# Kernel optimization log

Measured on AMD Instinct MI355X. Metric: run time of the kernel, lower is better.

## Reference

```python
import jax, jax.numpy as jnp
import numpy as np
import math

B, QL, HID = 4, 4, 4096          # batch, speculative q_len, hidden_size
NH, NKV, HD = 32, 8, 128         # attention heads, kv heads, head_dim
GROUPS = NH // NKV               # GQA repeat factor = 4
PRIOR = 4096                     # cached (prior) KV length
THETA = 1.0e6                    # Mixtral rope_theta


def setup_inputs() -> dict:
    key = jax.random.key(0)
    ks = jax.random.split(key, 7)
    hidden_states = jax.random.normal(ks[0], (B, QL, HID), jnp.float32)
    past_k = jax.random.normal(ks[1], (B, NKV, PRIOR, HD), jnp.float32)
    past_v = jax.random.normal(ks[2], (B, NKV, PRIOR, HD), jnp.float32)
    wq = jax.random.normal(ks[3], (HID, NH * HD), jnp.float32) * 0.02
    wk = jax.random.normal(ks[4], (HID, NKV * HD), jnp.float32) * 0.02
    wv = jax.random.normal(ks[5], (HID, NKV * HD), jnp.float32) * 0.02
    wo = jax.random.normal(ks[6], (NH * HD, HID), jnp.float32) * 0.02
    # prior mask: all cached positions visible
    attention_mask = jnp.ones((B, 1, QL, PRIOR), dtype=bool)
    # active mask: causal over the speculative window
    active_mask = jnp.broadcast_to(jnp.tril(jnp.ones((QL, QL), dtype=bool)), (B, 1, QL, QL))
    position_ids = jnp.broadcast_to(PRIOR + jnp.arange(QL, dtype=jnp.int64), (B, QL))
    return {"hidden_states": hidden_states, "past_k": past_k, "past_v": past_v,
            "wq": wq, "wk": wk, "wv": wv, "wo": wo,
            "attention_mask": attention_mask, "active_mask": active_mask,
            "position_ids": position_ids}


def _rotate_half(x):
    x1, x2 = jnp.split(x, 2, axis=-1)
    return jnp.concatenate([-x2, x1], axis=-1)


def _rope_cos_sin(position_ids):
    inv_freq = 1.0 / (THETA ** (jnp.arange(0, HD, 2, dtype=jnp.float32) / HD))  # [HD/2]
    freqs = position_ids.astype(jnp.float32)[..., None] * inv_freq              # [B,QL,HD/2]
    emb = jnp.concatenate([freqs, freqs], axis=-1)                              # [B,QL,HD]
    return jnp.cos(emb)[:, None], jnp.sin(emb)[:, None]                          # [B,1,QL,HD]


def reference(hidden_states, past_k, past_v, wq, wk, wv, wo,
              attention_mask, active_mask, position_ids):
    # fused QKV projection (no bias in Mixtral)
    q = (hidden_states @ wq).reshape(B, QL, NH, HD).transpose(0, 2, 1, 3)   # [B,NH,QL,HD]
    k = (hidden_states @ wk).reshape(B, QL, NKV, HD).transpose(0, 2, 1, 3)  # [B,NKV,QL,HD]
    v = (hidden_states @ wv).reshape(B, QL, NKV, HD).transpose(0, 2, 1, 3)
    # RoPE on Q and active K
    cos, sin = _rope_cos_sin(position_ids)
    q = q * cos + _rotate_half(q) * sin
    k = k * cos + _rotate_half(k) * sin
    # GQA repeat_kv
    k_prior = jnp.repeat(past_k, GROUPS, axis=1)  # [B,NH,PRIOR,HD]
    v_prior = jnp.repeat(past_v, GROUPS, axis=1)
    k_active = jnp.repeat(k, GROUPS, axis=1)      # [B,NH,QL,HD]
    v_active = jnp.repeat(v, GROUPS, axis=1)
    scale = 1.0 / math.sqrt(HD)
    neg = jnp.finfo(jnp.float32).min
    prior_scores = jnp.einsum('bhqd,bhkd->bhqk', q, k_prior) * scale
    prior_scores = jnp.where(attention_mask, prior_scores, neg)
    active_scores = jnp.einsum('bhqd,bhkd->bhqk', q, k_active) * scale
    active_scores = jnp.where(active_mask, active_scores, neg)   # is_speculation=True
    # decomposed softmax: shared max and shared divisor across prior/active
    max_score = jnp.maximum(prior_scores.max(-1, keepdims=True),
                            active_scores.max(-1, keepdims=True))
    prior_exp = jnp.exp(prior_scores - max_score)
    active_exp = jnp.exp(active_scores - max_score)
    divisor = prior_exp.sum(-1, keepdims=True) + active_exp.sum(-1, keepdims=True)
    attn = (jnp.einsum('bhqk,bhkd->bhqd', prior_exp / divisor, v_prior) +
            jnp.einsum('bhqk,bhkd->bhqd', active_exp / divisor, v_active))
    attn = attn.transpose(0, 2, 1, 3).reshape(B, QL, NH * HD)
    return attn @ wo
```

## Files before the change

### kernel.cpp

```cpp
#include <hip/hip_runtime.h>
#include <math.h>

#define NROWS 16
#define NCOLS 6144
#define HID   4096
#define NKV   8
#define HD    128
#define PRIOR 4096
#define NCH   32
#define CHUNK 128
#define SUB   64
#define KCQ   64
#define NKCQ  64
#define KCO   64
#define NKCO  64

__device__ __forceinline__ float rdlane(float v, int l) {
    return __int_as_float(__builtin_amdgcn_readlane(__float_as_int(v), l));
}

__global__ __launch_bounds__(128)
void k_qkv_partial(const float* __restrict__ hid,
                   const float* __restrict__ wq,
                   const float* __restrict__ wk,
                   const float* __restrict__ wv,
                   float* __restrict__ part)
{
    const int t   = threadIdx.x;
    const int col = blockIdx.x * 256 + t * 2;
    const int kc  = blockIdx.y;
    const int k0  = kc * KCQ;
    const float* w; int wn, wcol;
    if (col < 4096)      { w = wq; wn = 4096; wcol = col; }
    else if (col < 5120) { w = wk; wn = 1024; wcol = col - 4096; }
    else                 { w = wv; wn = 1024; wcol = col - 5120; }
    const float* wp = w + wcol + (size_t)k0 * wn;

    float acc[NROWS][2];
#pragma unroll
    for (int m = 0; m < NROWS; m++) { acc[m][0] = 0.f; acc[m][1] = 0.f; }
#pragma unroll 4
    for (int kk = 0; kk < KCQ; kk += 4) {
        const float2 w0 = *(const float2*)(wp + (size_t)(kk + 0) * wn);
        const float2 w1 = *(const float2*)(wp + (size_t)(kk + 1) * wn);
        const float2 w2 = *(const float2*)(wp + (size_t)(kk + 2) * wn);
        const float2 w3 = *(const float2*)(wp + (size_t)(kk + 3) * wn);
#pragma unroll
        for (int m = 0; m < NROWS; m++) {
            const float4 h4 = *(const float4*)(hid + (size_t)m * HID + k0 + kk);
            acc[m][0] = fmaf(h4.x, w0.x, fmaf(h4.y, w1.x, fmaf(h4.z, w2.x, fmaf(h4.w, w3.x, acc[m][0]))));
            acc[m][1] = fmaf(h4.x, w0.y, fmaf(h4.y, w1.y, fmaf(h4.z, w2.y, fmaf(h4.w, w3.y, acc[m][1]))));
        }
    }
    float* po = part + (size_t)kc * (NROWS * NCOLS) + col;
#pragma unroll
    for (int m = 0; m < NROWS; m++)
        *(float2*)(po + (size_t)m * NCOLS) = make_float2(acc[m][0], acc[m][1]);
}

__global__ __launch_bounds__(256)
void k_reduce_rope(const float* __restrict__ part, float* __restrict__ qkv)
{
    const int tid  = blockIdx.x * 256 + threadIdx.x;
    const int w    = tid >> 6, lane = tid & 63;
    const int u    = w * 16 + (lane & 15);
    const int sub  = lane >> 4;
    const int cs   = sub * 16;
    const double L64 = 0.21586735246819178;

    if (u < 32768) {
        const int d = u & 63, h = (u >> 6) & 31, r = u >> 11;
        const int c1 = h * HD + d;
        float s1 = 0.f, s2 = 0.f;
#pragma unroll 8
        for (int i = 0; i < 16; i++) {
            const float* p = part + (size_t)(cs + i) * (NROWS * NCOLS) + r * NCOLS + c1;
            s1 += p[0]; s2 += p[64];
        }
        s1 += __shfl_xor(s1, 16); s1 += __shfl_xor(s1, 32);
        s2 += __shfl_xor(s2, 16); s2 += __shfl_xor(s2, 32);
        if (sub == 0) {
            const double ang = (double)(PRIOR + (r & 3)) * exp(-(double)d * L64);
            double sv, cv; sincos(ang, &sv, &cv);
            const float cf = (float)cv, sf = (float)sv, sc = 0.08838834764831845f;
            qkv[r * NCOLS + c1]      = (s1 * cf - s2 * sf) * sc;
            qkv[r * NCOLS + c1 + 64] = (s2 * cf + s1 * sf) * sc;
        }
    } else if (u < 40960) {
        const int idx = u - 32768;
        const int d = idx & 63, kh = (idx >> 6) & 7, r = idx >> 9;
        const int c1 = 4096 + kh * HD + d;
        float s1 = 0.f, s2 = 0.f;
#pragma unroll 8
        for (int i = 0; i < 16; i++) {
            const float* p = part + (size_t)(cs + i) * (NROWS * NCOLS) + r * NCOLS + c1;
            s1 += p[0]; s2 += p[64];
        }
        s1 += __shfl_xor(s1, 16); s1 += __shfl_xor(s1, 32);
        s2 += __shfl_xor(s2, 16); s2 += __shfl_xor(s2, 32);
        if (sub == 0) {
            const double ang = (double)(PRIOR + (r & 3)) * exp(-(double)d * L64);
            double sv, cv; sincos(ang, &sv, &cv);
            const float cf = (float)cv, sf = (float)sv;
            qkv[r * NCOLS + c1]      = s1 * cf - s2 * sf;
            qkv[r * NCOLS + c1 + 64] = s2 * cf + s1 * sf;
        }
    } else {
        const int idx = u - 40960;
        const int n = idx & 1023, r = idx >> 10;
        const int c1 = 5120 + n;
        float s = 0.f;
#pragma unroll 8
        for (int i = 0; i < 16; i++)
            s += part[(size_t)(cs + i) * (NROWS * NCOLS) + r * NCOLS + c1];
        s += __shfl_xor(s, 16); s += __shfl_xor(s, 32);
        if (sub == 0) qkv[r * NCOLS + c1] = s;
    }
}

__global__ __launch_bounds__(256, 4)
void k_attn_prior(const float* __restrict__ qkv,
                  const float* __restrict__ pk,
                  const float* __restrict__ pv,
                  float* __restrict__ part3)
{
    const int chunk = blockIdx.x, kvh = blockIdx.y, b = blockIdx.z;
    const int t = threadIdx.x;
    const int lane = t & 63;

    __shared__ float kT[128][64];
    __shared__ float qT[128][16];

    const int qt = t >> 6;
    const int h  = (lane >> 4) & 3;
    const int kt = lane & 15;

    const size_t kvoff = ((size_t)(b * NKV + kvh) * PRIOR + (size_t)chunk * CHUNK) * HD;
    const float* kbase = pk + kvoff;
    const float* vbase = pv + kvoff;

    float4 kreg[8];
    {
        const float* kr = kbase + (size_t)lane * HD + qt * 32;
#pragma unroll
        for (int i = 0; i < 8; i++) kreg[i] = *(const float4*)(kr + i * 4);
    }

    for (int i = t; i < 2048; i += 256) {
        const int r = i & 15, d = i >> 4;
        const int ql = r & 3, g = r >> 2;
        qT[d][r] = qkv[(size_t)(b * 4 + ql) * NCOLS + (kvh * 4 + g) * HD + d];
    }

    float m_r[4], l_r[4], o[4][2];
#pragma unroll
    for (int i = 0; i < 4; i++) { m_r[i] = -INFINITY; l_r[i] = 0.f; o[i][0] = 0.f; o[i][1] = 0.f; }

    for (int st = 0; st < CHUNK / SUB; st++) {
#pragma unroll
        for (int i = 0; i < 8; i++) {
            const int d = qt * 32 + i * 4;
            kT[d + 0][lane] = kreg[i].x; kT[d + 1][lane] = kreg[i].y;
            kT[d + 2][lane] = kreg[i].z; kT[d + 3][lane] = kreg[i].w;
        }
        if (st == 0) {
            const float* kr = kbase + (size_t)(SUB + lane) * HD + qt * 32;
#pragma unroll
            for (int i = 0; i < 8; i++) kreg[i] = *(const float4*)(kr + i * 4);
        }
        __syncthreads();

        float a[4][4];
#pragma unroll
        for (int i = 0; i < 4; i++)
#pragma unroll
            for (int j = 0; j < 4; j++) a[i][j] = 0.f;
#pragma unroll 4
        for (int dd = 0; dd < 32; dd++) {
            const int d = h * 32 + dd;
            const float4 q4 = *(const float4*)(&qT[d][qt * 4]);
            const float4 k4 = *(const float4*)(&kT[d][kt * 4]);
            a[0][0]=fmaf(q4.x,k4.x,a[0][0]); a[0][1]=fmaf(q4.x,k4.y,a[0][1]); a[0][2]=fmaf(q4.x,k4.z,a[0][2]); a[0][3]=fmaf(q4.x,k4.w,a[0][3]);
            a[1][0]=fmaf(q4.y,k4.x,a[1][0]); a[1][1]=fmaf(q4.y,k4.y,a[1][1]); a[1][2]=fmaf(q4.y,k4.z,a[1][2]); a[1][3]=fmaf(q4.y,k4.w,a[1][3]);
            a[2][0]=fmaf(q4.z,k4.x,a[2][0]); a[2][1]=fmaf(q4.z,k4.y,a[2][1]); a[2][2]=fmaf(q4.z,k4.z,a[2][2]); a[2][3]=fmaf(q4.z,k4.w,a[2][3]);
            a[3][0]=fmaf(q4.w,k4.x,a[3][0]); a[3][1]=fmaf(q4.w,k4.y,a[3][1]); a[3][2]=fmaf(q4.w,k4.z,a[3][2]); a[3][3]=fmaf(q4.w,k4.w,a[3][3]);
        }
        __syncthreads();

        const float* vs = vbase + (size_t)st * SUB * HD + (lane << 1);
        float2 vb[4][4];
#pragma unroll
        for (int g = 0; g < 4; ++g)
#pragma unroll
            for (int j = 0; j < 4; ++j)
                vb[g][j] = *(const float2*)(vs + (size_t)(g * 4 + j) * HD);

#pragma unroll
        for (int i = 0; i < 4; i++)
#pragma unroll
            for (int j = 0; j < 4; j++) {
                float v = a[i][j];
                v += __shfl_xor(v, 16);
                v += __shfl_xor(v, 32);
                a[i][j] = v;
            }
        float al[4], pr[4][4];
#pragma unroll
        for (int i = 0; i < 4; i++) {
            float mx = fmaxf(fmaxf(a[i][0], a[i][1]), fmaxf(a[i][2], a[i][3]));
            mx = fmaxf(mx, __shfl_xor(mx, 1));
            mx = fmaxf(mx, __shfl_xor(mx, 2));
            mx = fmaxf(mx, __shfl_xor(mx, 4));
            mx = fmaxf(mx, __shfl_xor(mx, 8));
            const float mn = fmaxf(m_r[i], mx);
            al[i] = __expf(m_r[i] - mn);
            m_r[i] = mn;
            float s = 0.f;
#pragma unroll
            for (int j = 0; j < 4; j++) { pr[i][j] = __expf(a[i][j] - mn); s += pr[i][j]; }
            s += __shfl_xor(s, 1); s += __shfl_xor(s, 2);
            s += __shfl_xor(s, 4); s += __shfl_xor(s, 8);
            l_r[i] = l_r[i] * al[i] + s;
        }
#pragma unroll
        for (int i = 0; i < 4; i++) { o[i][0] *= al[i]; o[i][1] *= al[i]; }

#pragma unroll
        for (int g4 = 0; g4 < 16; ++g4) {
            const float2 v0 = vb[g4 & 3][0];
            const float2 v1 = vb[g4 & 3][1];
            const float2 v2 = vb[g4 & 3][2];
            const float2 v3 = vb[g4 & 3][3];
            if (g4 < 12) {
#pragma unroll
                for (int j = 0; j < 4; ++j)
                    vb[g4 & 3][j] = *(const float2*)(vs + (size_t)((g4 + 4) * 4 + j) * HD);
            }
#pragma unroll
            for (int i = 0; i < 4; i++) {
                const float p0 = rdlane(pr[i][0], g4);
                const float p1 = rdlane(pr[i][1], g4);
                const float p2 = rdlane(pr[i][2], g4);
                const float p3v = rdlane(pr[i][3], g4);
                o[i][0] = fmaf(p0,  v0.x, o[i][0]); o[i][1] = fmaf(p0,  v0.y, o[i][1]);
                o[i][0] = fmaf(p1,  v1.x, o[i][0]); o[i][1] = fmaf(p1,  v1.y, o[i][1]);
                o[i][0] = fmaf(p2,  v2.x, o[i][0]); o[i][1] = fmaf(p2,  v2.y, o[i][1]);
                o[i][0] = fmaf(p3v, v3.x, o[i][0]); o[i][1] = fmaf(p3v, v3.y, o[i][1]);
            }
        }
    }

    float* pout = part3 + (size_t)((b * NKV + kvh) * NCH + chunk) * 2080;
    if (lane == 0) {
#pragma unroll
        for (int i = 0; i < 4; i++) { pout[qt * 4 + i] = m_r[i]; pout[16 + qt * 4 + i] = l_r[i]; }
    }
#pragma unroll
    for (int i = 0; i < 4; i++)
        *(float2*)(pout + 32 + (size_t)(qt * 4 + i) * HD + (lane << 1)) =
            make_float2(o[i][0], o[i][1]);
}

__global__ __launch_bounds__(128)
void k_combine(const float* __restrict__ qkv,
               const float* __restrict__ part3,
               float* __restrict__ attn)
{
    const int bid = blockIdx.x;
    const int hr = bid & 1, g = (bid >> 1) & 3, kvh = (bid >> 3) & 7, b = bid >> 6;
    const int t = threadIdx.x;
    const int lr0 = hr * 2, lr1 = lr0 + 1;
    __shared__ float qL[2][128], kA[4][128], vA[4][128];
    __shared__ float mC[NCH][2], lC[NCH][2], fC[NCH][2];
    __shared__ float sAct[2][4], pA[2][4], invL[2];

    for (int i = t; i < 256; i += 128) {
        const int lrl = i >> 7, d = i & 127;
        qL[lrl][d] = qkv[(size_t)(b * 4 + lr0 + lrl) * NCOLS + (kvh * 4 + g) * HD + d];
    }
    for (int i = t; i < 512; i += 128) {
        const int ql = i >> 7, d = i & 127;
        kA[ql][d] = qkv[(size_t)(b * 4 + ql) * NCOLS + 4096 + kvh * HD + d];
        vA[ql][d] = qkv[(size_t)(b * 4 + ql) * NCOLS + 5120 + kvh * HD + d];
    }
    const float* p3 = part3 + (size_t)(b * NKV + kvh) * NCH * 2080;
    for (int i = t; i < NCH * 2; i += 128) {
        const int c = i >> 1, lrl = i & 1;
        mC[c][lrl] = p3[c * 2080 + g * 4 + lr0 + lrl];
        lC[c][lrl] = p3[c * 2080 + 16 + g * 4 + lr0 + lrl];
    }
    __syncthreads();
    if (t < 64) {
        const int pp = t >> 3, dd = t & 7;
        const int lrl = pp >> 2, k = pp & 3;
        float s = 0.f;
#pragma unroll
        for (int d = 0; d < 16; d++)
            s = fmaf(qL[lrl][dd * 16 + d], kA[k][dd * 16 + d], s);
        s += __shfl_xor(s, 1); s += __shfl_xor(s, 2); s += __shfl_xor(s, 4);
        if (dd == 0) sAct[lrl][k] = s;
    }
    __syncthreads();
    if (t < 64) {
        const int lrl = t >> 5, c = t & 31;
        const int lr = lr0 + lrl;
        const float m  = mC[c][lrl];
        const bool act = (c < 4) && (c <= lr);
        const float sa = act ? sAct[lrl][c] : -INFINITY;
        float M = fmaxf(m, sa);
        M = fmaxf(M, __shfl_xor(M, 1));
        M = fmaxf(M, __shfl_xor(M, 2));
        M = fmaxf(M, __shfl_xor(M, 4));
        M = fmaxf(M, __shfl_xor(M, 8));
        M = fmaxf(M, __shfl_xor(M, 16));
        const float f = __expf(m - M);
        fC[c][lrl] = f;
        const float pact = act ? __expf(sa - M) : 0.f;
        if (c < 4) pA[lrl][c] = pact;
        float l = fmaf(f, lC[c][lrl], pact);
        l += __shfl_xor(l, 1); l += __shfl_xor(l, 2);
        l += __shfl_xor(l, 4); l += __shfl_xor(l, 8); l += __shfl_xor(l, 16);
        if (c == 0) invL[lrl] = 1.f / l;
    }
    __syncthreads();

    const int d = t;
    float o0 = 0.f, o1 = 0.f;
#pragma unroll 4
    for (int c = 0; c < NCH; c++) {
        const float* pa = p3 + c * 2080 + 32 + (g * 4 + lr0) * HD + d;
        o0 = fmaf(fC[c][0], pa[0],  o0);
        o1 = fmaf(fC[c][1], pa[HD], o1);
    }
#pragma unroll
    for (int k = 0; k < 4; k++) {
        const float v = vA[k][d];
        o0 = fmaf(pA[0][k], v, o0);
        o1 = fmaf(pA[1][k], v, o1);
    }
    attn[(size_t)(b * 4 + lr0) * HID + (kvh * 4 + g) * HD + d] = o0 * invL[0];
    attn[(size_t)(b * 4 + lr1) * HID + (kvh * 4 + g) * HD + d] = o1 * invL[1];
}

__global__ __launch_bounds__(128)
void k_out_partial(const float* __restrict__ attn,
                   const float* __restrict__ wo,
                   float* __restrict__ part)
{
    const int t = threadIdx.x;
    const int col = blockIdx.x * 256 + t * 2;
    const int kc = blockIdx.y;
    const int k0 = kc * KCO;
    const float* wp = wo + col + (size_t)k0 * HID;

    float acc[NROWS][2];
#pragma unroll
    for (int m = 0; m < NROWS; m++) { acc[m][0] = 0.f; acc[m][1] = 0.f; }
#pragma unroll 4
    for (int kk = 0; kk < KCO; kk += 4) {
        const float2 w0 = *(const float2*)(wp + (size_t)(kk + 0) * HID);
        const float2 w1 = *(const float2*)(wp + (size_t)(kk + 1) * HID);
        const float2 w2 = *(const float2*)(wp + (size_t)(kk + 2) * HID);
        const float2 w3 = *(const float2*)(wp + (size_t)(kk + 3) * HID);
#pragma unroll
        for (int m = 0; m < NROWS; m++) {
            const float4 h4 = *(const float4*)(attn + (size_t)m * HID + k0 + kk);
            acc[m][0] = fmaf(h4.x, w0.x, fmaf(h4.y, w1.x, fmaf(h4.z, w2.x, fmaf(h4.w, w3.x, acc[m][0]))));
            acc[m][1] = fmaf(h4.x, w0.y, fmaf(h4.y, w1.y, fmaf(h4.z, w2.y, fmaf(h4.w, w3.y, acc[m][1]))));
        }
    }
    float* po = part + (size_t)kc * (NROWS * HID) + col;
#pragma unroll
    for (int m = 0; m < NROWS; m++)
        *(float2*)(po + (size_t)m * HID) = make_float2(acc[m][0], acc[m][1]);
}

__global__ __launch_bounds__(256)
void k_out_reduce(const float* __restrict__ part, float* __restrict__ out)
{
    const int tid = blockIdx.x * 256 + threadIdx.x;
    const int w = tid >> 6, lane = tid & 63;
    const int oid = w * 16 + (lane & 15);
    const int sub = lane >> 4;
    const float* p = part + (size_t)oid * 4 + (size_t)(sub * 16) * (NROWS * HID);
    float4 s = make_float4(0.f, 0.f, 0.f, 0.f);
#pragma unroll 8
    for (int c = 0; c < 16; c++) {
        const float4 a = *(const float4*)(p + (size_t)c * (NROWS * HID));
        s.x += a.x; s.y += a.y; s.z += a.z; s.w += a.w;
    }
    s.x += __shfl_xor(s.x, 16); s.x += __shfl_xor(s.x, 32);
    s.y += __shfl_xor(s.y, 16); s.y += __shfl_xor(s.y, 32);
    s.z += __shfl_xor(s.z, 16); s.z += __shfl_xor(s.z, 32);
    s.w += __shfl_xor(s.w, 16); s.w += __shfl_xor(s.w, 32);
    if (sub == 0) *(float4*)(out + (size_t)oid * 4) = s;
}

extern "C" void kernel_launch(void* const* d_in, const int* in_sizes, int n_in,
                              void* d_out, int out_size, void* d_ws, size_t ws_size,
                              hipStream_t stream)
{
    (void)in_sizes; (void)n_in; (void)out_size; (void)ws_size;
    const float* hid = (const float*)d_in[0];
    const float* pk  = (const float*)d_in[1];
    const float* pv  = (const float*)d_in[2];
    const float* wq  = (const float*)d_in[3];
    const float* wk  = (const float*)d_in[4];
    const float* wv  = (const float*)d_in[5];
    const float* wo  = (const float*)d_in[6];
    float* out = (float*)d_out;
    float* ws  = (float*)d_ws;

    float* P1   = ws;
    float* P3   = ws;
    float* P5   = ws;
    float* qkv  = ws + 6291456;
    float* attn = ws + 6389760;

    k_qkv_partial<<<dim3(24, NKCQ), 128, 0, stream>>>(hid, wq, wk, wv, P1);
    k_reduce_rope<<<896, 256, 0, stream>>>(P1, qkv);
    k_attn_prior<<<dim3(NCH, NKV, 4), 256, 0, stream>>>(qkv, pk, pv, P3);
    k_combine<<<256, 128, 0, stream>>>(qkv, P3, attn);
    k_out_partial<<<dim3(16, NKCO), 128, 0, stream>>>(attn, wo, P5);
    k_out_reduce<<<256, 256, 0, stream>>>(P5, out);
}
```

Baseline: 314.9 us.

## Widen reduction kernels, prefetch V before QK, double combine threads

The two split-K reduction kernels now use 16 lanes per output with 4 partial sums each instead of 4 lanes with 16, launching four times as many blocks. The V loads in the prior-attention loop are issued before the barrier and QK dot product so their latency overlaps the compute. The combine kernel uses 256 threads, one per (row, dim), instead of 128 threads each handling two rows. Together these aim to expose more memory-level parallelism in latency-bound stages, at the cost of extra shuffles and more live registers during the QK loop.

```diff
diff --git a/kernel.cpp b/kernel.cpp
--- a/kernel.cpp
+++ b/kernel.cpp
@@ -63,21 +63,23 @@
 {
     const int tid  = blockIdx.x * 256 + threadIdx.x;
     const int w    = tid >> 6, lane = tid & 63;
-    const int u    = w * 16 + (lane & 15);
-    const int sub  = lane >> 4;
-    const int cs   = sub * 16;
+    const int u    = w * 4 + (lane & 3);
+    const int sub  = lane >> 2;
+    const int cs   = sub * 4;
     const double L64 = 0.21586735246819178;
 
     if (u < 32768) {
         const int d = u & 63, h = (u >> 6) & 31, r = u >> 11;
         const int c1 = h * HD + d;
         float s1 = 0.f, s2 = 0.f;
-#pragma unroll 8
-        for (int i = 0; i < 16; i++) {
+#pragma unroll
+        for (int i = 0; i < 4; i++) {
             const float* p = part + (size_t)(cs + i) * (NROWS * NCOLS) + r * NCOLS + c1;
             s1 += p[0]; s2 += p[64];
         }
+        s1 += __shfl_xor(s1, 4); s1 += __shfl_xor(s1, 8);
         s1 += __shfl_xor(s1, 16); s1 += __shfl_xor(s1, 32);
+        s2 += __shfl_xor(s2, 4); s2 += __shfl_xor(s2, 8);
         s2 += __shfl_xor(s2, 16); s2 += __shfl_xor(s2, 32);
         if (sub == 0) {
             const double ang = (double)(PRIOR + (r & 3)) * exp(-(double)d * L64);
@@ -91,12 +93,14 @@
         const int d = idx & 63, kh = (idx >> 6) & 7, r = idx >> 9;
         const int c1 = 4096 + kh * HD + d;
         float s1 = 0.f, s2 = 0.f;
-#pragma unroll 8
-        for (int i = 0; i < 16; i++) {
+#pragma unroll
+        for (int i = 0; i < 4; i++) {
             const float* p = part + (size_t)(cs + i) * (NROWS * NCOLS) + r * NCOLS + c1;
             s1 += p[0]; s2 += p[64];
         }
+        s1 += __shfl_xor(s1, 4); s1 += __shfl_xor(s1, 8);
         s1 += __shfl_xor(s1, 16); s1 += __shfl_xor(s1, 32);
+        s2 += __shfl_xor(s2, 4); s2 += __shfl_xor(s2, 8);
         s2 += __shfl_xor(s2, 16); s2 += __shfl_xor(s2, 32);
         if (sub == 0) {
             const double ang = (double)(PRIOR + (r & 3)) * exp(-(double)d * L64);
@@ -110,9 +114,10 @@
         const int n = idx & 1023, r = idx >> 10;
         const int c1 = 5120 + n;
         float s = 0.f;
-#pragma unroll 8
-        for (int i = 0; i < 16; i++)
+#pragma unroll
+        for (int i = 0; i < 4; i++)
             s += part[(size_t)(cs + i) * (NROWS * NCOLS) + r * NCOLS + c1];
+        s += __shfl_xor(s, 4); s += __shfl_xor(s, 8);
         s += __shfl_xor(s, 16); s += __shfl_xor(s, 32);
         if (sub == 0) qkv[r * NCOLS + c1] = s;
     }
@@ -168,6 +173,15 @@
 #pragma unroll
             for (int i = 0; i < 8; i++) kreg[i] = *(const float4*)(kr + i * 4);
         }
+
+        const float* vs = vbase + (size_t)st * SUB * HD + (lane << 1);
+        float2 vb[4][4];
+#pragma unroll
+        for (int g = 0; g < 4; ++g)
+#pragma unroll
+            for (int j = 0; j < 4; ++j)
+                vb[g][j] = *(const float2*)(vs + (size_t)(g * 4 + j) * HD);
+
         __syncthreads();
 
         float a[4][4];
@@ -187,14 +201,6 @@
         }
         __syncthreads();
 
-        const float* vs = vbase + (size_t)st * SUB * HD + (lane << 1);
-        float2 vb[4][4];
-#pragma unroll
-        for (int g = 0; g < 4; ++g)
-#pragma unroll
-            for (int j = 0; j < 4; ++j)
-                vb[g][j] = *(const float2*)(vs + (size_t)(g * 4 + j) * HD);
-
 #pragma unroll
         for (int i = 0; i < 4; i++)
 #pragma unroll
@@ -261,7 +267,7 @@
             make_float2(o[i][0], o[i][1]);
 }
 
-__global__ __launch_bounds__(128)
+__global__ __launch_bounds__(256)
 void k_combine(const float* __restrict__ qkv,
                const float* __restrict__ part3,
                float* __restrict__ attn)
@@ -274,18 +280,18 @@
     __shared__ float mC[NCH][2], lC[NCH][2], fC[NCH][2];
     __shared__ float sAct[2][4], pA[2][4], invL[2];
 
-    for (int i = t; i < 256; i += 128) {
-        const int lrl = i >> 7, d = i & 127;
+    if (t < 256) {
+        const int lrl = t >> 7, d = t & 127;
         qL[lrl][d] = qkv[(size_t)(b * 4 + lr0 + lrl) * NCOLS + (kvh * 4 + g) * HD + d];
     }
-    for (int i = t; i < 512; i += 128) {
+    for (int i = t; i < 512; i += 256) {
         const int ql = i >> 7, d = i & 127;
         kA[ql][d] = qkv[(size_t)(b * 4 + ql) * NCOLS + 4096 + kvh * HD + d];
         vA[ql][d] = qkv[(size_t)(b * 4 + ql) * NCOLS + 5120 + kvh * HD + d];
     }
     const float* p3 = part3 + (size_t)(b * NKV + kvh) * NCH * 2080;
-    for (int i = t; i < NCH * 2; i += 128) {
-        const int c = i >> 1, lrl = i & 1;
+    if (t < NCH * 2) {
+        const int c = t >> 1, lrl = t & 1;
         mC[c][lrl] = p3[c * 2080 + g * 4 + lr0 + lrl];
         lC[c][lrl] = p3[c * 2080 + 16 + g * 4 + lr0 + lrl];
     }
@@ -324,22 +330,15 @@
     }
     __syncthreads();
 
-    const int d = t;
-    float o0 = 0.f, o1 = 0.f;
+    const int d = t & 127, lrl = t >> 7;
+    float o = 0.f;
 #pragma unroll 4
-    for (int c = 0; c < NCH; c++) {
-        const float* pa = p3 + c * 2080 + 32 + (g * 4 + lr0) * HD + d;
-        o0 = fmaf(fC[c][0], pa[0],  o0);
-        o1 = fmaf(fC[c][1], pa[HD], o1);
-    }
-#pragma unroll
-    for (int k = 0; k < 4; k++) {
-        const float v = vA[k][d];
-        o0 = fmaf(pA[0][k], v, o0);
-        o1 = fmaf(pA[1][k], v, o1);
-    }
-    attn[(size_t)(b * 4 + lr0) * HID + (kvh * 4 + g) * HD + d] = o0 * invL[0];
-    attn[(size_t)(b * 4 + lr1) * HID + (kvh * 4 + g) * HD + d] = o1 * invL[1];
+    for (int c = 0; c < NCH; c++)
+        o = fmaf(fC[c][lrl], p3[c * 2080 + 32 + (size_t)(g * 4 + lr0 + lrl) * HD + d], o);
+#pragma unroll
+    for (int k = 0; k < 4; k++)
+        o = fmaf(pA[lrl][k], vA[k][d], o);
+    attn[(size_t)(b * 4 + lr0 + lrl) * HID + (kvh * 4 + g) * HD + d] = o * invL[lrl];
 }
 
 __global__ __launch_bounds__(128)
@@ -380,18 +379,22 @@
 {
     const int tid = blockIdx.x * 256 + threadIdx.x;
     const int w = tid >> 6, lane = tid & 63;
-    const int oid = w * 16 + (lane & 15);
-    const int sub = lane >> 4;
-    const float* p = part + (size_t)oid * 4 + (size_t)(sub * 16) * (NROWS * HID);
+    const int oid = w * 4 + (lane & 3);
+    const int sub = lane >> 2;
+    const float* p = part + (size_t)oid * 4 + (size_t)(sub * 4) * (NROWS * HID);
     float4 s = make_float4(0.f, 0.f, 0.f, 0.f);
-#pragma unroll 8
-    for (int c = 0; c < 16; c++) {
+#pragma unroll
+    for (int c = 0; c < 4; c++) {
         const float4 a = *(const float4*)(p + (size_t)c * (NROWS * HID));
         s.x += a.x; s.y += a.y; s.z += a.z; s.w += a.w;
     }
+    s.x += __shfl_xor(s.x, 4); s.x += __shfl_xor(s.x, 8);
     s.x += __shfl_xor(s.x, 16); s.x += __shfl_xor(s.x, 32);
+    s.y += __shfl_xor(s.y, 4); s.y += __shfl_xor(s.y, 8);
     s.y += __shfl_xor(s.y, 16); s.y += __shfl_xor(s.y, 32);
+    s.z += __shfl_xor(s.z, 4); s.z += __shfl_xor(s.z, 8);
     s.z += __shfl_xor(s.z, 16); s.z += __shfl_xor(s.z, 32);
+    s.w += __shfl_xor(s.w, 4); s.w += __shfl_xor(s.w, 8);
     s.w += __shfl_xor(s.w, 16); s.w += __shfl_xor(s.w, 32);
     if (sub == 0) *(float4*)(out + (size_t)oid * 4) = s;
 }
@@ -418,9 +421,9 @@
     float* attn = ws + 6389760;
 
     k_qkv_partial<<<dim3(24, NKCQ), 128, 0, stream>>>(hid, wq, wk, wv, P1);
-    k_reduce_rope<<<896, 256, 0, stream>>>(P1, qkv);
+    k_reduce_rope<<<3584, 256, 0, stream>>>(P1, qkv);
     k_attn_prior<<<dim3(NCH, NKV, 4), 256, 0, stream>>>(qkv, pk, pv, P3);
-    k_combine<<<256, 128, 0, stream>>>(qkv, P3, attn);
+    k_combine<<<256, 256, 0, stream>>>(qkv, P3, attn);
     k_out_partial<<<dim3(16, NKCO), 128, 0, stream>>>(attn, wo, P5);
-    k_out_reduce<<<256, 256, 0, stream>>>(P5, out);
-}
+    k_out_reduce<<<1024, 256, 0, stream>>>(P5, out);
+}
```

New measurement: 324.6 us. +3.1%, slower.
